# Kernel optimization log

Measured on AMD Instinct MI355X. Metric: run time of the kernel, lower is better.

## Reference

```python
import jax, jax.numpy as jnp
import numpy as np

H = 16   # num_heads
K = 2    # top_k experts per token


def _layer_norm(x, g, b, eps=1e-5):
    mu = jnp.mean(x, axis=-1, keepdims=True)
    var = jnp.mean(jnp.square(x - mu), axis=-1, keepdims=True)
    return (x - mu) * jax.lax.rsqrt(var + eps) * g + b


def setup_inputs() -> dict:
    key = jax.random.key(0)
    ks = jax.random.split(key, 8)
    B, S, D, E = 2, 2048, 1024, 8
    sc = 0.02
    return {
        "x": jax.random.normal(ks[0], (B, S, D), jnp.float32),
        "wq": jax.random.normal(ks[1], (D, D), jnp.float32) * sc,
        "wk": jax.random.normal(ks[2], (D, D), jnp.float32) * sc,
        "wv": jax.random.normal(ks[3], (D, D), jnp.float32) * sc,
        "wo": jax.random.normal(ks[4], (D, D), jnp.float32) * sc,
        "ln1_g": jnp.ones((D,), jnp.float32),
        "ln1_b": jnp.zeros((D,), jnp.float32),
        "ln2_g": jnp.ones((D,), jnp.float32),
        "ln2_b": jnp.zeros((D,), jnp.float32),
        "router_w": jax.random.normal(ks[5], (E, D), jnp.float32) * sc,
        "expert_w": jax.random.normal(ks[6], (E, D, D), jnp.float32) * sc,
    }


def reference(x, wq, wk, wv, wo, ln1_g, ln1_b, ln2_g, ln2_b, router_w, expert_w):
    B, S, D = x.shape
    E = expert_w.shape[0]
    hd = D // H

    # ---- attention sublayer: x = x + attn(norm1(x)) ----
    h = _layer_norm(x, ln1_g, ln1_b)
    q = (h @ wq.T).reshape(B, S, H, hd).transpose(0, 2, 1, 3)  # bhsd
    k = (h @ wk.T).reshape(B, S, H, hd).transpose(0, 2, 1, 3)
    v = (h @ wv.T).reshape(B, S, H, hd).transpose(0, 2, 1, 3)
    scores = jnp.einsum("bhqd,bhkd->bhqk", q, k) / jnp.sqrt(jnp.float32(hd))
    causal = jnp.tril(jnp.ones((S, S), dtype=bool))
    scores = jnp.where(causal, scores, jnp.finfo(scores.dtype).min)
    probs = jax.nn.softmax(scores, axis=-1)
    attn = jnp.einsum("bhqk,bhkd->bhqd", probs, v)
    attn = attn.transpose(0, 2, 1, 3).reshape(B, S, D) @ wo.T
    x = x + attn

    # ---- MoE sublayer: x = x + moe(norm2(x)) ----
    h2 = _layer_norm(x, ln2_g, ln2_b)
    logits = jnp.einsum("bsd,ed->bse", h2, router_w)          # [B,S,E]
    top_logits, top_ids = jax.lax.top_k(logits, K)            # [B,S,K]
    gates = jax.nn.softmax(top_logits, axis=-1)               # [B,S,K]
    # dense combine weights over experts (E is small): sum_k gate_k * onehot(id_k)
    combine = jnp.sum(jax.nn.one_hot(top_ids, E, dtype=h2.dtype) * gates[..., None], axis=-2)  # [B,S,E]
    # per-token matvec with expert weights: token @ W_e.T for each expert, then weighted sum
    y = jnp.einsum("bsd,eod->bseo", h2, expert_w)             # [B,S,E,D]
    moe_out = jnp.einsum("bse,bseo->bso", combine, y)
    return x + moe_out
```

## Files before the change

### kernel.cpp

```cpp
#include <hip/hip_runtime.h>
#include <hip/hip_bf16.h>
#include <cstdint>


typedef __bf16 bf16;
typedef __bf16 bf16x8 __attribute__((ext_vector_type(8)));
typedef __bf16 bf16x4 __attribute__((ext_vector_type(4)));
typedef float f32x4 __attribute__((ext_vector_type(4)));
typedef float f32x16 __attribute__((ext_vector_type(16)));

#define MFMA(a, b, c) __builtin_amdgcn_mfma_f32_16x16x32_bf16(a, b, c, 0, 0, 0)
#define MFMA32(a, b, c) __builtin_amdgcn_mfma_f32_32x32x16_bf16(a, b, c, 0, 0, 0)

__device__ __forceinline__ void gld16(void* lds, const void* g) {
  __builtin_amdgcn_global_load_lds(
      (const __attribute__((address_space(1))) void*)g,
      (__attribute__((address_space(3))) void*)lds, 16, 0, 0);
}

__global__ void prep_weights(const float* __restrict__ wq, const float* __restrict__ wk,
                             const float* __restrict__ wv, const float* __restrict__ wo,
                             const float* __restrict__ expw,
                             bf16* __restrict__ wqh, bf16* __restrict__ wql,
                             bf16* __restrict__ wkh, bf16* __restrict__ wkl,
                             bf16* __restrict__ wvh,
                             bf16* __restrict__ woh, bf16* __restrict__ wol,
                             bf16* __restrict__ ewh) {
  int bid = blockIdx.x;
  if (bid < 4096) {
    int wsel = bid >> 10;
    const float* src = wsel == 0 ? wq : wsel == 1 ? wk : wsel == 2 ? wv : wo;
    bf16* hi = wsel == 0 ? wqh : wsel == 1 ? wkh : wsel == 2 ? wvh : woh;
    bf16* lo = wsel == 0 ? wql : wsel == 1 ? wkl : wsel == 2 ? (bf16*)nullptr : wol;
    int i = ((bid & 1023) * 256 + threadIdx.x) * 4;
    float4 v = *(const float4*)(src + i);
    float a[4] = {v.x, v.y, v.z, v.w};
#pragma unroll
    for (int j = 0; j < 4; j++) {
      bf16 h = (bf16)a[j];
      hi[i + j] = h;
      if (wsel != 2) lo[i + j] = (bf16)(a[j] - (float)h);
    }
  } else {
    int i = ((bid - 4096) * 256 + threadIdx.x) * 4;
    float4 v = *(const float4*)(expw + i);
    ewh[i] = (bf16)v.x; ewh[i + 1] = (bf16)v.y;
    ewh[i + 2] = (bf16)v.z; ewh[i + 3] = (bf16)v.w;
  }
}

__global__ void ln_split(const float* __restrict__ x, const float* __restrict__ g,
                         const float* __restrict__ b, bf16* __restrict__ hi,
                         bf16* __restrict__ lo) {
  int tok = blockIdx.x, t = threadIdx.x;
  float4 v = ((const float4*)(x + (size_t)tok * 1024))[t];
  float s = v.x + v.y + v.z + v.w;
  float ss = v.x * v.x + v.y * v.y + v.z * v.z + v.w * v.w;
#pragma unroll
  for (int o = 1; o < 64; o <<= 1) { s += __shfl_xor(s, o); ss += __shfl_xor(ss, o); }
  __shared__ float red[8];
  int w = t >> 6, lane = t & 63;
  if (lane == 0) { red[w] = s; red[4 + w] = ss; }
  __syncthreads();
  s = red[0] + red[1] + red[2] + red[3];
  ss = red[4] + red[5] + red[6] + red[7];
  float mu = s * (1.f / 1024.f);
  float rstd = rsqrtf(ss * (1.f / 1024.f) - mu * mu + 1e-5f);
  float4 gv = ((const float4*)g)[t], bv = ((const float4*)b)[t];
  float y[4] = {(v.x - mu) * rstd * gv.x + bv.x, (v.y - mu) * rstd * gv.y + bv.y,
                (v.z - mu) * rstd * gv.z + bv.z, (v.w - mu) * rstd * gv.w + bv.w};
  size_t o = (size_t)tok * 1024 + t * 4;
#pragma unroll
  for (int j = 0; j < 4; j++) {
    bf16 h = (bf16)y[j];
    hi[o + j] = h;
    lo[o + j] = (bf16)(y[j] - (float)h);
  }
}

__global__ void ln2route(const float* __restrict__ x1, const float* __restrict__ g,
                         const float* __restrict__ b, const float* __restrict__ rw,
                         bf16* __restrict__ h2h, int* __restrict__ eid,
                         float2* __restrict__ gout) {
  int tok = blockIdx.x, t = threadIdx.x;
  float4 v = ((const float4*)(x1 + (size_t)tok * 1024))[t];
  float s = v.x + v.y + v.z + v.w;
  float ss = v.x * v.x + v.y * v.y + v.z * v.z + v.w * v.w;
#pragma unroll
  for (int o = 1; o < 64; o <<= 1) { s += __shfl_xor(s, o); ss += __shfl_xor(ss, o); }
  __shared__ float red[8];
  __shared__ float h2s[1024];
  __shared__ float lg[8];
  int w = t >> 6, lane = t & 63;
  if (lane == 0) { red[w] = s; red[4 + w] = ss; }
  __syncthreads();
  s = red[0] + red[1] + red[2] + red[3];
  ss = red[4] + red[5] + red[6] + red[7];
  float mu = s * (1.f / 1024.f);
  float rstd = rsqrtf(ss * (1.f / 1024.f) - mu * mu + 1e-5f);
  float4 gv = ((const float4*)g)[t], bv = ((const float4*)b)[t];
  float4 y;
  y.x = (v.x - mu) * rstd * gv.x + bv.x;
  y.y = (v.y - mu) * rstd * gv.y + bv.y;
  y.z = (v.z - mu) * rstd * gv.z + bv.z;
  y.w = (v.w - mu) * rstd * gv.w + bv.w;
  ((float4*)h2s)[t] = y;
  size_t o = (size_t)tok * 1024 + t * 4;
  h2h[o] = (bf16)y.x; h2h[o + 1] = (bf16)y.y;
  h2h[o + 2] = (bf16)y.z; h2h[o + 3] = (bf16)y.w;
  __syncthreads();
  float a0 = 0.f, a1 = 0.f;
  const float4* r0 = (const float4*)(rw + (2 * w) * 1024);
  const float4* r1 = (const float4*)(rw + (2 * w + 1) * 1024);
#pragma unroll
  for (int it = 0; it < 4; it++) {
    float4 xv = ((const float4*)h2s)[lane + 64 * it];
    float4 w0 = r0[lane + 64 * it];
    float4 w1 = r1[lane + 64 * it];
    a0 += xv.x * w0.x + xv.y * w0.y + xv.z * w0.z + xv.w * w0.w;
    a1 += xv.x * w1.x + xv.y * w1.y + xv.z * w1.z + xv.w * w1.w;
  }
#pragma unroll
  for (int o2 = 1; o2 < 64; o2 <<= 1) {
    a0 += __shfl_xor(a0, o2);
    a1 += __shfl_xor(a1, o2);
  }
  if (lane == 0) { lg[2 * w] = a0; lg[2 * w + 1] = a1; }
  __syncthreads();
  if (t == 0) {
    int i0 = 0; float l0 = lg[0];
#pragma unroll
    for (int e = 1; e < 8; e++) if (lg[e] > l0) { l0 = lg[e]; i0 = e; }
    int i1 = -1; float l1 = -3e38f;
#pragma unroll
    for (int e = 0; e < 8; e++) if (e != i0 && lg[e] > l1) { l1 = lg[e]; i1 = e; }
    float e1 = __expf(l1 - l0);
    float den = 1.f + e1;
    eid[tok] = i0 | (i1 << 4);
    gout[tok] = make_float2(1.f / den, e1 / den);
  }
}

__global__ void build_lists(const int* __restrict__ eid,
                            const float2* __restrict__ gv,
                            int* __restrict__ tlist, float* __restrict__ glist,
                            int* __restrict__ cnt) {
  int e = blockIdx.x, t = threadIdx.x;
  int lane = t & 63, w = t >> 6;
  __shared__ int wt[4];
  int base = 0;
  for (int c = 0; c < 16; c++) {
    int tok = c * 256 + t;
    int pair = eid[tok];
    int e0 = pair & 15, e1 = pair >> 4;
    bool p = (e0 == e) || (e1 == e);
    float2 g2 = gv[tok];
    float gate = (e0 == e) ? g2.x : g2.y;
    unsigned long long m = __ballot(p);
    int rank = __popcll(m & ((1ull << lane) - 1ull));
    if (lane == 0) wt[w] = __popcll(m);
    __syncthreads();
    int off = base;
    for (int i = 0; i < w; i++) off += wt[i];
    if (p) {
      tlist[e * 4096 + off + rank] = tok;
      glist[e * 4096 + off + rank] = gate;
    }
    base += wt[0] + wt[1] + wt[2] + wt[3];
    __syncthreads();
  }
  if (t == 0) cnt[e] = base;
  int pad = (base + 127) & ~127;
  if (pad > 4096) pad = 4096;
  for (int i = base + t; i < pad; i += 256) {
    tlist[e * 4096 + i] = 0;
    glist[e * 4096 + i] = 0.f;
  }
}

__device__ __forceinline__ void gemm_core_split(
    const bf16* __restrict__ Ah, const bf16* __restrict__ Al,
    const bf16* __restrict__ Bh, const bf16* __restrict__ Bl, int m0, int n0,
    f32x4 (&acc)[4][4]) {
  __shared__ __align__(16) bf16 As_h[4096], As_l[4096], Bs_h[4096], Bs_l[4096];
  int t = threadIdx.x, lane = t & 63, w = t >> 6;
  int i0 = t, i1 = t + 256;
  const bf16* a0h = Ah + (size_t)(m0 + (i0 >> 2)) * 1024 + (i0 & 3) * 8;
  const bf16* a1h = Ah + (size_t)(m0 + (i1 >> 2)) * 1024 + (i1 & 3) * 8;
  const bf16* a0l = Al + (size_t)(m0 + (i0 >> 2)) * 1024 + (i0 & 3) * 8;
  const bf16* a1l = Al + (size_t)(m0 + (i1 >> 2)) * 1024 + (i1 & 3) * 8;
  const bf16* b0h = Bh + (size_t)(n0 + (i0 >> 2)) * 1024 + (i0 & 3) * 8;
  const bf16* b1h = Bh + (size_t)(n0 + (i1 >> 2)) * 1024 + (i1 & 3) * 8;
  const bf16* b0l = Bl + (size_t)(n0 + (i0 >> 2)) * 1024 + (i0 & 3) * 8;
  const bf16* b1l = Bl + (size_t)(n0 + (i1 >> 2)) * 1024 + (i1 & 3) * 8;
  int wm = (w >> 1) * 64, wn = (w & 1) * 64;
  int lr = lane & 15, lq = lane >> 4;
  for (int k0 = 0; k0 < 1024; k0 += 32) {
    __syncthreads();
    gld16(&As_h[i0 * 8], a0h + k0); gld16(&As_h[i1 * 8], a1h + k0);
    gld16(&As_l[i0 * 8], a0l + k0); gld16(&As_l[i1 * 8], a1l + k0);
    gld16(&Bs_h[i0 * 8], b0h + k0); gld16(&Bs_h[i1 * 8], b1h + k0);
    gld16(&Bs_l[i0 * 8], b0l + k0); gld16(&Bs_l[i1 * 8], b1l + k0);
    __syncthreads();
    bf16x8 ah[4], al4[4], bh[4], bl4[4];
#pragma unroll
    for (int i = 0; i < 4; i++) {
      ah[i]  = *(const bf16x8*)&As_h[(wm + i * 16 + lr) * 32 + lq * 8];
      al4[i] = *(const bf16x8*)&As_l[(wm + i * 16 + lr) * 32 + lq * 8];
      bh[i]  = *(const bf16x8*)&Bs_h[(wn + i * 16 + lr) * 32 + lq * 8];
      bl4[i] = *(const bf16x8*)&Bs_l[(wn + i * 16 + lr) * 32 + lq * 8];
    }
#pragma unroll
    for (int i = 0; i < 4; i++)
#pragma unroll
      for (int j = 0; j < 4; j++) {
        f32x4 c = acc[i][j];
        c = MFMA(ah[i], bh[j], c);
        c = MFMA(ah[i], bl4[j], c);
        c = MFMA(al4[i], bh[j], c);
        acc[i][j] = c;
      }
  }
}

__global__ __launch_bounds__(256, 2) void gemm_qk(
    const bf16* __restrict__ hh, const bf16* __restrict__ hl,
    const bf16* __restrict__ wqh, const bf16* __restrict__ wql,
    const bf16* __restrict__ wkh, const bf16* __restrict__ wkl,
    bf16* __restrict__ qh, bf16* __restrict__ ql, bf16* __restrict__ kh,
    bf16* __restrict__ kl) {
  int n0 = blockIdx.x * 128, m0 = blockIdx.y * 128, z = blockIdx.z;
  const bf16* Bh = z ? wkh : wqh;
  const bf16* Bl = z ? wkl : wql;
  f32x4 acc[4][4];
#pragma unroll
  for (int i = 0; i < 4; i++)
#pragma unroll
    for (int j = 0; j < 4; j++) acc[i][j] = (f32x4){0.f, 0.f, 0.f, 0.f};
  gemm_core_split(hh, hl, Bh, Bl, m0, n0, acc);
  int t = threadIdx.x, lane = t & 63, w = t >> 6;
  int wm = (w >> 1) * 64, wn = (w & 1) * 64, lr = lane & 15, lq = lane >> 4;
  bf16* Oh = z ? kh : qh;
  bf16* Ol = z ? kl : ql;
  float scale = z ? 1.0f : (0.125f * 1.44269504f);
#pragma unroll
  for (int i = 0; i < 4; i++)
#pragma unroll
    for (int j = 0; j < 4; j++)
#pragma unroll
      for (int r = 0; r < 4; r++) {
        size_t row = m0 + wm + i * 16 + lq * 4 + r;
        int col = n0 + wn + j * 16 + lr;
        float v = acc[i][j][r] * scale;
        bf16 h = (bf16)v;
        Oh[row * 1024 + col] = h;
        Ol[row * 1024 + col] = (bf16)(v - (float)h);
      }
}

__global__ __launch_bounds__(256, 2) void gemm_v(
    const bf16* __restrict__ A, const bf16* __restrict__ B,
    bf16* __restrict__ vth) {
  int n0 = blockIdx.x * 128, m0 = blockIdx.y * 128;
  __shared__ __align__(16) bf16 As[4096], Bs[4096];
  int t = threadIdx.x, lane = t & 63, w = t >> 6;
  int i0 = t, i1 = t + 256;
  const bf16* a0 = A + (size_t)(m0 + (i0 >> 2)) * 1024 + (i0 & 3) * 8;
  const bf16* a1 = A + (size_t)(m0 + (i1 >> 2)) * 1024 + (i1 & 3) * 8;
  const bf16* b0 = B + (size_t)(n0 + (i0 >> 2)) * 1024 + (i0 & 3) * 8;
  const bf16* b1 = B + (size_t)(n0 + (i1 >> 2)) * 1024 + (i1 & 3) * 8;
  int wm = (w >> 1) * 64, wn = (w & 1) * 64, lr = lane & 15, lq = lane >> 4;
  f32x4 acc[4][4];
#pragma unroll
  for (int i = 0; i < 4; i++)
#pragma unroll
    for (int j = 0; j < 4; j++) acc[i][j] = (f32x4){0.f, 0.f, 0.f, 0.f};
  for (int k0 = 0; k0 < 1024; k0 += 32) {
    __syncthreads();
    gld16(&As[i0 * 8], a0 + k0); gld16(&As[i1 * 8], a1 + k0);
    gld16(&Bs[i0 * 8], b0 + k0); gld16(&Bs[i1 * 8], b1 + k0);
    __syncthreads();
    bf16x8 af[4], bfr[4];
#pragma unroll
    for (int i = 0; i < 4; i++) {
      af[i] = *(const bf16x8*)&As[(wm + i * 16 + lr) * 32 + lq * 8];
      bfr[i] = *(const bf16x8*)&Bs[(wn + i * 16 + lr) * 32 + lq * 8];
    }
#pragma unroll
    for (int i = 0; i < 4; i++)
#pragma unroll
      for (int j = 0; j < 4; j++) acc[i][j] = MFMA(af[i], bfr[j], acc[i][j]);
  }
  int bb = m0 >> 11;
  int srow0 = m0 & 2047;
#pragma unroll
  for (int i = 0; i < 4; i++)
#pragma unroll
    for (int j = 0; j < 4; j++) {
      int col = n0 + wn + j * 16 + lr;
      int head = col >> 6, d = col & 63;
      int s = srow0 + wm + i * 16 + lq * 4;
      int ss = (s & ~63) | (((((s >> 2) & 15)) ^ (d & 15)) << 2);
      bf16x4 hv;
#pragma unroll
      for (int r = 0; r < 4; r++) hv[r] = (bf16)acc[i][j][r];
      size_t off = ((size_t)((bb * 16 + head) * 64 + d)) * 2048 + ss;
      *(bf16x4*)(vth + off) = hv;
    }
}

__global__ __launch_bounds__(256, 2) void gemm_wo(
    const float* __restrict__ Oacc, const float* __restrict__ Lacc,
    const bf16* __restrict__ bh, const bf16* __restrict__ bl,
    const float* __restrict__ resid, float* __restrict__ outp) {
  int n0 = blockIdx.x * 128, m0 = blockIdx.y * 128;
  __shared__ __align__(16) bf16 As_h[4096], As_l[4096], Bs_h[4096], Bs_l[4096];
  int t = threadIdx.x, lane = t & 63, w = t >> 6;
  int i0 = t, i1 = t + 256;
  int row0 = m0 + (i0 >> 2), row1 = m0 + (i1 >> 2);
  const float* a0 = Oacc + (size_t)row0 * 1024 + (i0 & 3) * 8;
  const float* a1 = Oacc + (size_t)row1 * 1024 + (i1 & 3) * 8;
  const bf16* b0h = bh + (size_t)(n0 + (i0 >> 2)) * 1024 + (i0 & 3) * 8;
  const bf16* b1h = bh + (size_t)(n0 + (i1 >> 2)) * 1024 + (i1 & 3) * 8;
  const bf16* b0l = bl + (size_t)(n0 + (i0 >> 2)) * 1024 + (i0 & 3) * 8;
  const bf16* b1l = bl + (size_t)(n0 + (i1 >> 2)) * 1024 + (i1 & 3) * 8;
  int wm = (w >> 1) * 64, wn = (w & 1) * 64;
  int lr = lane & 15, lq = lane >> 4;
  f32x4 acc[4][4];
#pragma unroll
  for (int i = 0; i < 4; i++)
#pragma unroll
    for (int j = 0; j < 4; j++) acc[i][j] = (f32x4){0.f, 0.f, 0.f, 0.f};
  for (int k0 = 0; k0 < 1024; k0 += 32) {
    __syncthreads();
    gld16(&Bs_h[i0 * 8], b0h + k0); gld16(&Bs_h[i1 * 8], b1h + k0);
    gld16(&Bs_l[i0 * 8], b0l + k0); gld16(&Bs_l[i1 * 8], b1l + k0);
    int hd = k0 >> 6;
    float linv0 = 1.f / Lacc[row0 * 16 + hd];
    float linv1 = 1.f / Lacc[row1 * 16 + hd];
    float4 va0 = *(const float4*)(a0 + k0);
    float4 vb0 = *(const float4*)(a0 + k0 + 4);
    float4 va1 = *(const float4*)(a1 + k0);
    float4 vb1 = *(const float4*)(a1 + k0 + 4);
    float f0[8] = {va0.x, va0.y, va0.z, va0.w, vb0.x, vb0.y, vb0.z, vb0.w};
    float f1[8] = {va1.x, va1.y, va1.z, va1.w, vb1.x, vb1.y, vb1.z, vb1.w};
    bf16x8 h0, l0, h1, l1;
#pragma unroll
    for (int j = 0; j < 8; j++) {
      float x0 = f0[j] * linv0;
      bf16 hh0 = (bf16)x0;
      h0[j] = hh0; l0[j] = (bf16)(x0 - (float)hh0);
      float x1 = f1[j] * linv1;
      bf16 hh1 = (bf16)x1;
      h1[j] = hh1; l1[j] = (bf16)(x1 - (float)hh1);
    }
    *(bf16x8*)&As_h[i0 * 8] = h0; *(bf16x8*)&As_l[i0 * 8] = l0;
    *(bf16x8*)&As_h[i1 * 8] = h1; *(bf16x8*)&As_l[i1 * 8] = l1;
    __syncthreads();
    bf16x8 ah[4], al4[4], bhf[4], bl4[4];
#pragma unroll
    for (int i = 0; i < 4; i++) {
      ah[i]  = *(const bf16x8*)&As_h[(wm + i * 16 + lr) * 32 + lq * 8];
      al4[i] = *(const bf16x8*)&As_l[(wm + i * 16 + lr) * 32 + lq * 8];
      bhf[i] = *(const bf16x8*)&Bs_h[(wn + i * 16 + lr) * 32 + lq * 8];
      bl4[i] = *(const bf16x8*)&Bs_l[(wn + i * 16 + lr) * 32 + lq * 8];
    }
#pragma unroll
    for (int i = 0; i < 4; i++)
#pragma unroll
      for (int j = 0; j < 4; j++) {
        f32x4 c = acc[i][j];
        c = MFMA(ah[i], bhf[j], c);
        c = MFMA(ah[i], bl4[j], c);
        c = MFMA(al4[i], bhf[j], c);
        acc[i][j] = c;
      }
  }
#pragma unroll
  for (int i = 0; i < 4; i++)
#pragma unroll
    for (int j = 0; j < 4; j++)
#pragma unroll
      for (int r = 0; r < 4; r++) {
        size_t row = m0 + wm + i * 16 + lq * 4 + r;
        int col = n0 + wn + j * 16 + lr;
        outp[row * 1024 + col] = resid[row * 1024 + col] + acc[i][j][r];
      }
}

__device__ __forceinline__ f32x16 qk_subtile(
    const bf16* __restrict__ Ks, const bf16* __restrict__ Kls, int keyr, int l5,
    const bf16x8 (&qfh)[4], const bf16x8 (&qfl)[4]) {
  f32x16 sA, sB;
#pragma unroll
  for (int r = 0; r < 16; r++) { sA[r] = 0.f; sB[r] = 0.f; }
#pragma unroll
  for (int c = 0; c < 4; c++) {
    int dg = ((2 * c + l5) ^ (keyr & 7)) * 8;
    bf16x8 kv = *(const bf16x8*)&Ks[keyr * 64 + dg];
    bf16x8 km = *(const bf16x8*)&Kls[keyr * 64 + dg];
    if (c < 2) {
      sA = MFMA32(kv, qfh[c], sA);
      sA = MFMA32(kv, qfl[c], sA);
      sA = MFMA32(km, qfh[c], sA);
    } else {
      sB = MFMA32(kv, qfh[c], sB);
      sB = MFMA32(kv, qfl[c], sB);
      sB = MFMA32(km, qfh[c], sB);
    }
  }
  return sA + sB;
}

__device__ __forceinline__ void exp_pack_pv(
    f32x16 sc, bool maskt, int kb0, int qg, int ktile,
    float& lsum, f32x16& O0, f32x16& O1,
    const bf16* __restrict__ Vs, int l31, int l5) {
  float pvv[16];
#pragma unroll
  for (int r = 0; r < 16; r++) {
    int cst = (r & 3) + 8 * (r >> 2);
    float sv = sc[r];
    if (maskt && (kb0 + cst > qg)) sv = -30000.f;
    float p = __builtin_amdgcn_exp2f(sv);
    pvv[r] = p;
    lsum += p;
  }
  uint32_t hw[4][2], lw[4][2];
#pragma unroll
  for (int o = 0; o < 4; o++)
#pragma unroll
    for (int j = 0; j < 2; j++) {
      int ra = 4 * o + 2 * j;
      bf16 h0 = (bf16)pvv[ra], h1 = (bf16)pvv[ra + 1];
      union { bf16 h[2]; uint32_t u; } ph, pl;
      ph.h[0] = h0; ph.h[1] = h1;
      pl.h[0] = (bf16)(pvv[ra] - (float)h0);
      pl.h[1] = (bf16)(pvv[ra + 1] - (float)h1);
      hw[o][j] = ph.u;
      lw[o][j] = pl.u;
    }
#pragma unroll
  for (int c2 = 0; c2 < 2; c2++) {
    union { uint32_t u[4]; bf16x8 v; } pa, plo;
    pa.u[0] = hw[2 * c2][0];     pa.u[1] = hw[2 * c2][1];
    pa.u[2] = hw[2 * c2 + 1][0]; pa.u[3] = hw[2 * c2 + 1][1];
    plo.u[0] = lw[2 * c2][0];     plo.u[1] = lw[2 * c2][1];
    plo.u[2] = lw[2 * c2 + 1][0]; plo.u[3] = lw[2 * c2 + 1][1];
    __builtin_amdgcn_s_setprio(1);
#pragma unroll
    for (int dtile = 0; dtile < 2; dtile++) {
      int d = dtile * 32 + l31;
      int pqA = ((8 * ktile + 4 * c2 + l5) ^ (d & 15)) * 4;
      union { bf16x4 q[2]; bf16x8 v; } vbu;
      vbu.q[0] = *(const bf16x4*)&Vs[d * 64 + pqA];
      vbu.q[1] = *(const bf16x4*)&Vs[d * 64 + (pqA ^ 8)];
      if (dtile == 0) {
        O0 = MFMA32(pa.v, vbu.v, O0);
        O0 = MFMA32(plo.v, vbu.v, O0);
      } else {
        O1 = MFMA32(pa.v, vbu.v, O1);
        O1 = MFMA32(plo.v, vbu.v, O1);
      }
    }
    __builtin_amdgcn_s_setprio(0);
  }
}

__global__ __launch_bounds__(256, 3) void attn_fused(
    const bf16* __restrict__ qh, const bf16* __restrict__ ql,
    const bf16* __restrict__ kh, const bf16* __restrict__ kl,
    const bf16* __restrict__ vth,
    float* __restrict__ O_acc, float* __restrict__ L_acc) {
  const int S = 2048, D = 1024;
  static const unsigned char QTt[40] = {
      15, 15, 15, 15, 14, 14, 14, 13, 13, 13, 12, 12, 12, 11, 11, 11,
      10, 10, 9, 9, 8, 8, 7, 7, 6, 5, 4, 3,
      14, 10, 6, 2, 13, 9, 5, 1, 12, 8, 4, 0};
  static const unsigned char C0t[40] = {
      0, 8, 16, 24, 0, 8, 16, 0, 8, 16, 0, 8, 16, 0, 8, 16,
      0, 8, 0, 8, 0, 8, 0, 8, 0, 0, 0, 0,
      24, 16, 8, 0, 24, 16, 8, 0, 24, 16, 8, 0};
  static const unsigned char C1t[40] = {
      8, 16, 24, 32, 8, 16, 24, 8, 16, 24, 8, 16, 24, 8, 16, 24,
      8, 16, 8, 16, 8, 16, 8, 16, 8, 8, 8, 8,
      30, 22, 14, 6, 28, 20, 12, 4, 26, 18, 10, 2};
  int y = blockIdx.y;
  int qt = QTt[y];
  int tile0 = C0t[y], tile1 = C1t[y];
  int hb = blockIdx.x;
  int head = hb & 15, b = hb >> 4;
  int qb = qt * 128;
  int t = threadIdx.x, lane = t & 63, w = t >> 6;
  int l31 = lane & 31, l5 = lane >> 5;
  int base = b * S, hcol = head * 64;

  __shared__ __align__(16) bf16 Kh_s[2][4096], Kl_s[2][4096];
  __shared__ __align__(16) bf16 Vh_s[2][4096];

  bf16x8 qfh[4], qfl[4];
  {
    const bf16* p1 = qh + (size_t)(base + qb + w * 32 + l31) * D + hcol + l5 * 8;
    const bf16* p2 = ql + (size_t)(base + qb + w * 32 + l31) * D + hcol + l5 * 8;
#pragma unroll
    for (int c = 0; c < 4; c++) {
      qfh[c] = *(const bf16x8*)(p1 + 16 * c);
      qfl[c] = *(const bf16x8*)(p2 + 16 * c);
    }
  }
  f32x16 O0, O1;
  float lsum = 0.f;
#pragma unroll
  for (int r = 0; r < 16; r++) { O0[r] = 0.f; O1[r] = 0.f; }

  int r0 = t >> 3, p0 = t & 7;
  int g0 = p0 ^ (r0 & 7);
  const bf16* k0hp = kh + (size_t)(base + r0) * D + hcol + g0 * 8;
  const bf16* k1hp = kh + (size_t)(base + 32 + r0) * D + hcol + g0 * 8;
  const bf16* k0lp = kl + (size_t)(base + r0) * D + hcol + g0 * 8;
  const bf16* k1lp = kl + (size_t)(base + 32 + r0) * D + hcol + g0 * 8;
  const bf16* v0hp = vth + (size_t)(hb * 64 + r0) * 2048 + p0 * 8;
  const bf16* v1hp = vth + (size_t)(hb * 64 + 32 + r0) * 2048 + p0 * 8;

  int qwmin = qb + w * 32;

#define STAGE(kts, bb) do { \
    gld16(&Kh_s[bb][t * 8], k0hp + (size_t)(kts) * D); \
    gld16(&Kh_s[bb][2048 + t * 8], k1hp + (size_t)(kts) * D); \
    gld16(&Kl_s[bb][t * 8], k0lp + (size_t)(kts) * D); \
    gld16(&Kl_s[bb][2048 + t * 8], k1lp + (size_t)(kts) * D); \
    gld16(&Vh_s[bb][t * 8], v0hp + (kts)); \
    gld16(&Vh_s[bb][2048 + t * 8], v1hp + (kts)); \
  } while (0)

  STAGE(tile0 * 64, tile0 & 1);
  __syncthreads();

  for (int ti = tile0; ti < tile1; ++ti) {
    int kt = ti * 64;
    int bb = ti & 1;
    if (ti + 1 < tile1) STAGE((ti + 1) * 64, bb ^ 1);
    const bf16* Ks = &Kh_s[bb][0];
    const bf16* Kls = &Kl_s[bb][0];
    const bf16* Vs = &Vh_s[bb][0];
    if (kt + 64 <= qb) {
      __builtin_amdgcn_s_setprio(1);
      f32x16 sc0 = qk_subtile(Ks, Kls, l31, l5, qfh, qfl);
      f32x16 sc1 = qk_subtile(Ks, Kls, 32 + l31, l5, qfh, qfl);
      __builtin_amdgcn_s_setprio(0);
      exp_pack_pv(sc0, false, 0, 0, 0, lsum, O0, O1, Vs, l31, l5);
      exp_pack_pv(sc1, false, 0, 0, 1, lsum, O0, O1, Vs, l31, l5);
    } else if (kt <= qwmin + 31) {
      bool skip1 = (kt + 32 > qwmin + 31);
#pragma unroll
      for (int ktile = 0; ktile < 2; ktile++) {
        if (ktile == 1 && skip1) break;
        bool maskt = (kt + 32 * ktile + 31 > qwmin);
        __builtin_amdgcn_s_setprio(1);
        f32x16 sc = qk_subtile(Ks, Kls, ktile * 32 + l31, l5, qfh, qfl);
        __builtin_amdgcn_s_setprio(0);
        int kb0 = kt + 32 * ktile + 4 * l5;
        int qg = qwmin + l31;
        exp_pack_pv(sc, maskt, kb0, qg, ktile, lsum, O0, O1, Vs, l31, l5);
      }
    }
    __syncthreads();
  }
#undef STAGE
  if (tile0 * 64 <= qwmin + 31) {
    float ltot = lsum + __shfl_xor(lsum, 32);
    if (l5 == 0) {
      size_t tokq = (size_t)(base + qb + w * 32 + l31);
      atomicAdd(&L_acc[tokq * 16 + head], ltot);
    }
#pragma unroll
    for (int r = 0; r < 16; r++) {
      int qlocal = (r & 3) + 8 * (r >> 2) + 4 * l5;
      size_t tok = (size_t)(base + qb + w * 32 + qlocal);
      atomicAdd(&O_acc[tok * 1024 + hcol + l31], O0[r]);
      atomicAdd(&O_acc[tok * 1024 + hcol + 32 + l31], O1[r]);
    }
  }
}

__global__ __launch_bounds__(256, 2) void gemm_moe(
    const bf16* __restrict__ A, const bf16* __restrict__ W,
    const int* __restrict__ tlist, const float* __restrict__ glist,
    const int* __restrict__ cnt, float* __restrict__ outp) {
  int e = blockIdx.z;
  int count = cnt[e];
  int m0 = blockIdx.y * 128;
  if (m0 >= count) return;
  int n0 = blockIdx.x * 128;
  const int* tl = tlist + e * 4096;
  const bf16* B = W + (size_t)e * 1024 * 1024;
  __shared__ __align__(16) bf16 As[4096], Bs[4096];
  int t = threadIdx.x, lane = t & 63, w = t >> 6;
  int i0 = t, i1 = t + 256;
  int ra = tl[m0 + (i0 >> 2)], rb = tl[m0 + (i1 >> 2)];
  const bf16* a0 = A + (size_t)ra * 1024 + (i0 & 3) * 8;
  const bf16* a1 = A + (size_t)rb * 1024 + (i1 & 3) * 8;
  const bf16* b0 = B + (size_t)(n0 + (i0 >> 2)) * 1024 + (i0 & 3) * 8;
  const bf16* b1 = B + (size_t)(n0 + (i1 >> 2)) * 1024 + (i1 & 3) * 8;
  int wm = (w >> 1) * 64, wn = (w & 1) * 64, lr = lane & 15, lq = lane >> 4;
  f32x4 acc[4][4];
#pragma unroll
  for (int i = 0; i < 4; i++)
#pragma unroll
    for (int j = 0; j < 4; j++) acc[i][j] = (f32x4){0.f, 0.f, 0.f, 0.f};
  for (int k0 = 0; k0 < 1024; k0 += 32) {
    __syncthreads();
    gld16(&As[i0 * 8], a0 + k0); gld16(&As[i1 * 8], a1 + k0);
    gld16(&Bs[i0 * 8], b0 + k0); gld16(&Bs[i1 * 8], b1 + k0);
    __syncthreads();
    bf16x8 af[4], bfr[4];
#pragma unroll
    for (int i = 0; i < 4; i++) {
      af[i] = *(const bf16x8*)&As[(wm + i * 16 + lr) * 32 + lq * 8];
      bfr[i] = *(const bf16x8*)&Bs[(wn + i * 16 + lr) * 32 + lq * 8];
    }
#pragma unroll
    for (int i = 0; i < 4; i++)
#pragma unroll
      for (int j = 0; j < 4; j++) acc[i][j] = MFMA(af[i], bfr[j], acc[i][j]);
  }
#pragma unroll
  for (int i = 0; i < 4; i++)
#pragma unroll
    for (int r = 0; r < 4; r++) {
      int slot = m0 + wm + i * 16 + lq * 4 + r;
      if (slot < count) {
        int tok = tl[slot];
        float gte = glist[e * 4096 + slot];
#pragma unroll
        for (int j = 0; j < 4; j++) {
          int col = n0 + wn + j * 16 + lr;
          atomicAdd(&outp[(size_t)tok * 1024 + col], gte * acc[i][j][r]);
        }
      }
    }
}

extern "C" void kernel_launch(void* const* d_in, const int* in_sizes, int n_in,
                              void* d_out, int out_size, void* d_ws, size_t ws_size,
                              hipStream_t stream) {
  (void)in_sizes; (void)n_in; (void)out_size; (void)ws_size;
  const float* x    = (const float*)d_in[0];
  const float* wq   = (const float*)d_in[1];
  const float* wk   = (const float*)d_in[2];
  const float* wv   = (const float*)d_in[3];
  const float* wo   = (const float*)d_in[4];
  const float* ln1g = (const float*)d_in[5];
  const float* ln1b = (const float*)d_in[6];
  const float* ln2g = (const float*)d_in[7];
  const float* ln2b = (const float*)d_in[8];
  const float* rw   = (const float*)d_in[9];
  const float* expw = (const float*)d_in[10];
  float* out = (float*)d_out;

  char* p = (char*)d_ws;
  auto take = [&](size_t bytes) -> char* {
    char* r = p;
    p += (bytes + 255) & ~(size_t)255;
    return r;
  };
  const size_t ND2 = 4096ull * 1024 * 2;
  const size_t WD2 = 1024ull * 1024 * 2;
  bf16* h_hi = (bf16*)take(ND2); bf16* h_lo = (bf16*)take(ND2);
  bf16* wqh = (bf16*)take(WD2); bf16* wql = (bf16*)take(WD2);
  bf16* wkh = (bf16*)take(WD2); bf16* wkl = (bf16*)take(WD2);
  bf16* wvh = (bf16*)take(WD2);
  bf16* woh = (bf16*)take(WD2); bf16* wol = (bf16*)take(WD2);
  bf16* q_hi = (bf16*)take(ND2); bf16* q_lo = (bf16*)take(ND2);
  bf16* k_hi = (bf16*)take(ND2); bf16* k_lo = (bf16*)take(ND2);
  bf16* vt_hi = (bf16*)take(ND2);
  bf16* h2h  = (bf16*)take(ND2);
  bf16* ewh  = (bf16*)take(8ull * 1024 * 1024 * 2);
  int*   tlist  = (int*)take(8ull * 4096 * 4);
  float* glist  = (float*)take(8ull * 4096 * 4);
  int*   cnt    = (int*)take(64);
  int*   reid   = (int*)take(4096 * 4);
  float2* rg    = (float2*)take(4096 * 8);
  float* O_acc  = (float*)take(4096ull * 1024 * 4);
  float* L_acc  = (float*)take(4096ull * 16 * 4);

  hipMemsetAsync(O_acc, 0, 4096ull * 1024 * 4, stream);
  hipMemsetAsync(L_acc, 0, 4096ull * 16 * 4, stream);
  prep_weights<<<12288, 256, 0, stream>>>(wq, wk, wv, wo, expw, wqh, wql, wkh,
                                          wkl, wvh, woh, wol, ewh);
  ln_split<<<4096, 256, 0, stream>>>(x, ln1g, ln1b, h_hi, h_lo);
  gemm_qk<<<dim3(8, 32, 2), 256, 0, stream>>>(h_hi, h_lo, wqh, wql, wkh, wkl,
                                              q_hi, q_lo, k_hi, k_lo);
  gemm_v<<<dim3(8, 32), 256, 0, stream>>>(h_hi, wvh, vt_hi);
  attn_fused<<<dim3(32, 40), 256, 0, stream>>>(q_hi, q_lo, k_hi, k_lo, vt_hi,
                                               O_acc, L_acc);
  gemm_wo<<<dim3(8, 32), 256, 0, stream>>>(O_acc, L_acc, woh, wol, x, out);
  ln2route<<<4096, 256, 0, stream>>>(out, ln2g, ln2b, rw, h2h, reid, rg);
  build_lists<<<8, 256, 0, stream>>>(reid, rg, tlist, glist, cnt);
  gemm_moe<<<dim3(8, 32, 8), 256, 0, stream>>>(h2h, ewh, tlist, glist, cnt,
                                               out);
}
```

Baseline: 415.0 us.

## Merge Q/K/V GEMMs into one launch and split-K the Wo projection

Folds the V projection into the Q/K GEMM launch as a third grid slice, raising launch_bounds occupancy to 3 and removing one kernel launch. The Wo GEMM is split along K into two halves that write fp32 partials into reused q/k buffers, which doubles its grid to fill more CUs. The residual add of x and the two partials moves into ln2route, which now also writes the residual stream. The two memsets are merged into one. This adds extra fp32 partial traffic and assumes the q/k buffers are large enough and no longer needed after attention.

After: 374.2 us (median of 3 runs). 9.8% less time.

```diff
diff --git a/kernel.cpp b/kernel.cpp
--- a/kernel.cpp
+++ b/kernel.cpp
@@ -78,12 +78,22 @@
   }
 }
 
-__global__ void ln2route(const float* __restrict__ x1, const float* __restrict__ g,
-                         const float* __restrict__ b, const float* __restrict__ rw,
+__global__ void ln2route(const float* __restrict__ x0,
+                         const float* __restrict__ P0, const float* __restrict__ P1,
+                         const float* __restrict__ g, const float* __restrict__ b,
+                         const float* __restrict__ rw, float* __restrict__ outp,
                          bf16* __restrict__ h2h, int* __restrict__ eid,
                          float2* __restrict__ gout) {
   int tok = blockIdx.x, t = threadIdx.x;
-  float4 v = ((const float4*)(x1 + (size_t)tok * 1024))[t];
+  float4 xv = ((const float4*)(x0 + (size_t)tok * 1024))[t];
+  float4 p0 = ((const float4*)(P0 + (size_t)tok * 1024))[t];
+  float4 p1 = ((const float4*)(P1 + (size_t)tok * 1024))[t];
+  float4 v;
+  v.x = xv.x + p0.x + p1.x;
+  v.y = xv.y + p0.y + p1.y;
+  v.z = xv.z + p0.z + p1.z;
+  v.w = xv.w + p0.w + p1.w;
+  ((float4*)(outp + (size_t)tok * 1024))[t] = v;
   float s = v.x + v.y + v.z + v.w;
   float ss = v.x * v.x + v.y * v.y + v.z * v.z + v.w * v.w;
 #pragma unroll
@@ -114,11 +124,11 @@
   const float4* r1 = (const float4*)(rw + (2 * w + 1) * 1024);
 #pragma unroll
   for (int it = 0; it < 4; it++) {
-    float4 xv = ((const float4*)h2s)[lane + 64 * it];
+    float4 xv2 = ((const float4*)h2s)[lane + 64 * it];
     float4 w0 = r0[lane + 64 * it];
     float4 w1 = r1[lane + 64 * it];
-    a0 += xv.x * w0.x + xv.y * w0.y + xv.z * w0.z + xv.w * w0.w;
-    a1 += xv.x * w1.x + xv.y * w1.y + xv.z * w1.z + xv.w * w1.w;
+    a0 += xv2.x * w0.x + xv2.y * w0.y + xv2.z * w0.z + xv2.w * w0.w;
+    a1 += xv2.x * w1.x + xv2.y * w1.y + xv2.z * w1.z + xv2.w * w1.w;
   }
 #pragma unroll
   for (int o2 = 1; o2 < 64; o2 <<= 1) {
@@ -223,97 +233,95 @@
   }
 }
 
-__global__ __launch_bounds__(256, 2) void gemm_qk(
+__global__ __launch_bounds__(256, 3) void gemm_qkv(
     const bf16* __restrict__ hh, const bf16* __restrict__ hl,
     const bf16* __restrict__ wqh, const bf16* __restrict__ wql,
     const bf16* __restrict__ wkh, const bf16* __restrict__ wkl,
+    const bf16* __restrict__ wvh,
     bf16* __restrict__ qh, bf16* __restrict__ ql, bf16* __restrict__ kh,
-    bf16* __restrict__ kl) {
+    bf16* __restrict__ kl, bf16* __restrict__ vth) {
   int n0 = blockIdx.x * 128, m0 = blockIdx.y * 128, z = blockIdx.z;
-  const bf16* Bh = z ? wkh : wqh;
-  const bf16* Bl = z ? wkl : wql;
-  f32x4 acc[4][4];
-#pragma unroll
-  for (int i = 0; i < 4; i++)
-#pragma unroll
-    for (int j = 0; j < 4; j++) acc[i][j] = (f32x4){0.f, 0.f, 0.f, 0.f};
-  gemm_core_split(hh, hl, Bh, Bl, m0, n0, acc);
   int t = threadIdx.x, lane = t & 63, w = t >> 6;
   int wm = (w >> 1) * 64, wn = (w & 1) * 64, lr = lane & 15, lq = lane >> 4;
-  bf16* Oh = z ? kh : qh;
-  bf16* Ol = z ? kl : ql;
-  float scale = z ? 1.0f : (0.125f * 1.44269504f);
-#pragma unroll
-  for (int i = 0; i < 4; i++)
-#pragma unroll
-    for (int j = 0; j < 4; j++)
-#pragma unroll
-      for (int r = 0; r < 4; r++) {
-        size_t row = m0 + wm + i * 16 + lq * 4 + r;
+  if (z < 2) {
+    const bf16* Bh = z ? wkh : wqh;
+    const bf16* Bl = z ? wkl : wql;
+    f32x4 acc[4][4];
+#pragma unroll
+    for (int i = 0; i < 4; i++)
+#pragma unroll
+      for (int j = 0; j < 4; j++) acc[i][j] = (f32x4){0.f, 0.f, 0.f, 0.f};
+    gemm_core_split(hh, hl, Bh, Bl, m0, n0, acc);
+    bf16* Oh = z ? kh : qh;
+    bf16* Ol = z ? kl : ql;
+    float scale = z ? 1.0f : (0.125f * 1.44269504f);
+#pragma unroll
+    for (int i = 0; i < 4; i++)
+#pragma unroll
+      for (int j = 0; j < 4; j++)
+#pragma unroll
+        for (int r = 0; r < 4; r++) {
+          size_t row = m0 + wm + i * 16 + lq * 4 + r;
+          int col = n0 + wn + j * 16 + lr;
+          float v = acc[i][j][r] * scale;
+          bf16 h = (bf16)v;
+          Oh[row * 1024 + col] = h;
+          Ol[row * 1024 + col] = (bf16)(v - (float)h);
+        }
+  } else {
+    __shared__ __align__(16) bf16 As[4096], Bs[4096];
+    int i0 = t, i1 = t + 256;
+    const bf16* a0 = hh + (size_t)(m0 + (i0 >> 2)) * 1024 + (i0 & 3) * 8;
+    const bf16* a1 = hh + (size_t)(m0 + (i1 >> 2)) * 1024 + (i1 & 3) * 8;
+    const bf16* b0 = wvh + (size_t)(n0 + (i0 >> 2)) * 1024 + (i0 & 3) * 8;
+    const bf16* b1 = wvh + (size_t)(n0 + (i1 >> 2)) * 1024 + (i1 & 3) * 8;
+    f32x4 acc[4][4];
+#pragma unroll
+    for (int i = 0; i < 4; i++)
+#pragma unroll
+      for (int j = 0; j < 4; j++) acc[i][j] = (f32x4){0.f, 0.f, 0.f, 0.f};
+    for (int k0 = 0; k0 < 1024; k0 += 32) {
+      __syncthreads();
+      gld16(&As[i0 * 8], a0 + k0); gld16(&As[i1 * 8], a1 + k0);
+      gld16(&Bs[i0 * 8], b0 + k0); gld16(&Bs[i1 * 8], b1 + k0);
+      __syncthreads();
+      bf16x8 af[4], bfr[4];
+#pragma unroll
+      for (int i = 0; i < 4; i++) {
+        af[i] = *(const bf16x8*)&As[(wm + i * 16 + lr) * 32 + lq * 8];
+        bfr[i] = *(const bf16x8*)&Bs[(wn + i * 16 + lr) * 32 + lq * 8];
+      }
+#pragma unroll
+      for (int i = 0; i < 4; i++)
+#pragma unroll
+        for (int j = 0; j < 4; j++) acc[i][j] = MFMA(af[i], bfr[j], acc[i][j]);
+    }
+    int bb = m0 >> 11;
+    int srow0 = m0 & 2047;
+#pragma unroll
+    for (int i = 0; i < 4; i++)
+#pragma unroll
+      for (int j = 0; j < 4; j++) {
         int col = n0 + wn + j * 16 + lr;
-        float v = acc[i][j][r] * scale;
-        bf16 h = (bf16)v;
-        Oh[row * 1024 + col] = h;
-        Ol[row * 1024 + col] = (bf16)(v - (float)h);
+        int head = col >> 6, d = col & 63;
+        int s = srow0 + wm + i * 16 + lq * 4;
+        int ss = (s & ~63) | (((((s >> 2) & 15)) ^ (d & 15)) << 2);
+        bf16x4 hv;
+#pragma unroll
+        for (int r = 0; r < 4; r++) hv[r] = (bf16)acc[i][j][r];
+        size_t off = ((size_t)((bb * 16 + head) * 64 + d)) * 2048 + ss;
+        *(bf16x4*)(vth + off) = hv;
       }
-}
-
-__global__ __launch_bounds__(256, 2) void gemm_v(
-    const bf16* __restrict__ A, const bf16* __restrict__ B,
-    bf16* __restrict__ vth) {
-  int n0 = blockIdx.x * 128, m0 = blockIdx.y * 128;
-  __shared__ __align__(16) bf16 As[4096], Bs[4096];
-  int t = threadIdx.x, lane = t & 63, w = t >> 6;
-  int i0 = t, i1 = t + 256;
-  const bf16* a0 = A + (size_t)(m0 + (i0 >> 2)) * 1024 + (i0 & 3) * 8;
-  const bf16* a1 = A + (size_t)(m0 + (i1 >> 2)) * 1024 + (i1 & 3) * 8;
-  const bf16* b0 = B + (size_t)(n0 + (i0 >> 2)) * 1024 + (i0 & 3) * 8;
-  const bf16* b1 = B + (size_t)(n0 + (i1 >> 2)) * 1024 + (i1 & 3) * 8;
-  int wm = (w >> 1) * 64, wn = (w & 1) * 64, lr = lane & 15, lq = lane >> 4;
-  f32x4 acc[4][4];
-#pragma unroll
-  for (int i = 0; i < 4; i++)
-#pragma unroll
-    for (int j = 0; j < 4; j++) acc[i][j] = (f32x4){0.f, 0.f, 0.f, 0.f};
-  for (int k0 = 0; k0 < 1024; k0 += 32) {
-    __syncthreads();
-    gld16(&As[i0 * 8], a0 + k0); gld16(&As[i1 * 8], a1 + k0);
-    gld16(&Bs[i0 * 8], b0 + k0); gld16(&Bs[i1 * 8], b1 + k0);
-    __syncthreads();
-    bf16x8 af[4], bfr[4];
-#pragma unroll
-    for (int i = 0; i < 4; i++) {
-      af[i] = *(const bf16x8*)&As[(wm + i * 16 + lr) * 32 + lq * 8];
-      bfr[i] = *(const bf16x8*)&Bs[(wn + i * 16 + lr) * 32 + lq * 8];
-    }
-#pragma unroll
-    for (int i = 0; i < 4; i++)
-#pragma unroll
-      for (int j = 0; j < 4; j++) acc[i][j] = MFMA(af[i], bfr[j], acc[i][j]);
-  }
-  int bb = m0 >> 11;
-  int srow0 = m0 & 2047;
-#pragma unroll
-  for (int i = 0; i < 4; i++)
-#pragma unroll
-    for (int j = 0; j < 4; j++) {
-      int col = n0 + wn + j * 16 + lr;
-      int head = col >> 6, d = col & 63;
-      int s = srow0 + wm + i * 16 + lq * 4;
-      int ss = (s & ~63) | (((((s >> 2) & 15)) ^ (d & 15)) << 2);
-      bf16x4 hv;
-#pragma unroll
-      for (int r = 0; r < 4; r++) hv[r] = (bf16)acc[i][j][r];
-      size_t off = ((size_t)((bb * 16 + head) * 64 + d)) * 2048 + ss;
-      *(bf16x4*)(vth + off) = hv;
-    }
+  }
 }
 
 __global__ __launch_bounds__(256, 2) void gemm_wo(
     const float* __restrict__ Oacc, const float* __restrict__ Lacc,
     const bf16* __restrict__ bh, const bf16* __restrict__ bl,
-    const float* __restrict__ resid, float* __restrict__ outp) {
-  int n0 = blockIdx.x * 128, m0 = blockIdx.y * 128;
+    float* __restrict__ P0, float* __restrict__ P1) {
+  int n0 = blockIdx.x * 128, m0 = blockIdx.y * 128, z = blockIdx.z;
+  float* P = z ? P1 : P0;
+  int kb = z * 512;
   __shared__ __align__(16) bf16 As_h[4096], As_l[4096], Bs_h[4096], Bs_l[4096];
   int t = threadIdx.x, lane = t & 63, w = t >> 6;
   int i0 = t, i1 = t + 256;
@@ -331,7 +339,7 @@
   for (int i = 0; i < 4; i++)
 #pragma unroll
     for (int j = 0; j < 4; j++) acc[i][j] = (f32x4){0.f, 0.f, 0.f, 0.f};
-  for (int k0 = 0; k0 < 1024; k0 += 32) {
+  for (int k0 = kb; k0 < kb + 512; k0 += 32) {
     __syncthreads();
     gld16(&Bs_h[i0 * 8], b0h + k0); gld16(&Bs_h[i1 * 8], b1h + k0);
     gld16(&Bs_l[i0 * 8], b0l + k0); gld16(&Bs_l[i1 * 8], b1l + k0);
@@ -384,7 +392,7 @@
       for (int r = 0; r < 4; r++) {
         size_t row = m0 + wm + i * 16 + lq * 4 + r;
         int col = n0 + wn + j * 16 + lr;
-        outp[row * 1024 + col] = resid[row * 1024 + col] + acc[i][j][r];
+        P[row * 1024 + col] = acc[i][j][r];
       }
 }
 
@@ -683,19 +691,21 @@
   float2* rg    = (float2*)take(4096 * 8);
   float* O_acc  = (float*)take(4096ull * 1024 * 4);
   float* L_acc  = (float*)take(4096ull * 16 * 4);
-
-  hipMemsetAsync(O_acc, 0, 4096ull * 1024 * 4, stream);
-  hipMemsetAsync(L_acc, 0, 4096ull * 16 * 4, stream);
+  float* P0 = (float*)q_hi;
+  float* P1 = (float*)k_hi;
+
+  hipMemsetAsync(O_acc, 0, 4096ull * 1024 * 4 + 4096ull * 16 * 4, stream);
   prep_weights<<<12288, 256, 0, stream>>>(wq, wk, wv, wo, expw, wqh, wql, wkh,
                                           wkl, wvh, woh, wol, ewh);
   ln_split<<<4096, 256, 0, stream>>>(x, ln1g, ln1b, h_hi, h_lo);
-  gemm_qk<<<dim3(8, 32, 2), 256, 0, stream>>>(h_hi, h_lo, wqh, wql, wkh, wkl,
-                                              q_hi, q_lo, k_hi, k_lo);
-  gemm_v<<<dim3(8, 32), 256, 0, stream>>>(h_hi, wvh, vt_hi);
+  gemm_qkv<<<dim3(8, 32, 3), 256, 0, stream>>>(h_hi, h_lo, wqh, wql, wkh, wkl,
+                                               wvh, q_hi, q_lo, k_hi, k_lo,
+                                               vt_hi);
   attn_fused<<<dim3(32, 40), 256, 0, stream>>>(q_hi, q_lo, k_hi, k_lo, vt_hi,
                                                O_acc, L_acc);
-  gemm_wo<<<dim3(8, 32), 256, 0, stream>>>(O_acc, L_acc, woh, wol, x, out);
-  ln2route<<<4096, 256, 0, stream>>>(out, ln2g, ln2b, rw, h2h, reid, rg);
+  gemm_wo<<<dim3(8, 32, 2), 256, 0, stream>>>(O_acc, L_acc, woh, wol, P0, P1);
+  ln2route<<<4096, 256, 0, stream>>>(x, P0, P1, ln2g, ln2b, rw, out, h2h,
+                                     reid, rg);
   build_lists<<<8, 256, 0, stream>>>(reid, rg, tlist, glist, cnt);
   gemm_moe<<<dim3(8, 32, 8), 256, 0, stream>>>(h2h, ewh, tlist, glist, cnt,
                                                out);
```
